# Kernel tuning notes

Hardware: AMD Instinct MI355X
Metric: run time of the kernel (lower is better)

Reference implementation:

```python
import jax, jax.numpy as jnp
import numpy as np

N_NODES = 100000
N_EDGES = 1200000
D = 64
GCN_LAYERS = 2
KEEP_PROB = 0.7


def setup_inputs() -> dict:
    key = jax.random.key(0)
    k1, k2, k3, k4, k5, k6, k7 = jax.random.split(key, 7)
    all_emb = jax.random.normal(k1, (N_NODES, D), dtype=jnp.float32)
    W = jax.random.normal(k2, (D, D), dtype=jnp.float32) * 0.05
    b = jax.random.normal(k3, (D,), dtype=jnp.float32) * 0.05
    # sparse adjacency values (e.g. normalized weights)
    vals = jax.random.uniform(k4, (N_EDGES,), dtype=jnp.float32)
    # per-layer dropout uniforms, mirrors torch.rand(len(values)) each layer
    drop_u = jax.random.uniform(k5, (GCN_LAYERS, N_EDGES), dtype=jnp.float32)
    rows = jax.random.randint(k6, (N_EDGES,), 0, N_NODES)
    cols = jax.random.randint(k7, (N_EDGES,), 0, N_NODES)
    return {"all_emb": all_emb, "W": W, "b": b, "vals": vals,
            "drop_u": drop_u, "rows": rows, "cols": cols}


def reference(all_emb, W, b, vals, drop_u, rows, cols):
    # emb[0] = fc(all_emb)
    acc = all_emb @ W.T + b  # [N, D]
    x = all_emb
    for layer in range(GCN_LAYERS):
        # edge dropout: keep iff (u + keep_prob) floors to 1, scale by 1/keep_prob
        keep = (drop_u[layer] + KEEP_PROB) >= 1.0
        v = jnp.where(keep, vals / KEEP_PROB, 0.0)  # [E]
        # SpMM: x <- A_dropped @ x via gather + segment-sum scatter
        msgs = v[:, None] * x[cols]  # [E, D]
        x = jax.ops.segment_sum(msgs, rows, num_segments=N_NODES)  # [N, D]
        acc = acc + x
    # mean over stacked (gcn_layers + 1) embeddings
    return acc / float(GCN_LAYERS + 1)
```

## Files before the change

kernel.cpp:

```cpp
#include <hip/hip_runtime.h>

#define N_NODES 100000
#define N_EDGES 1200000
#define D 64
#define KEEP_PROB 0.7f
#define INV_KEEP (1.0f / KEEP_PROB)
#define NBUCK 1564
#define MAXB 1024
#define PPART 256
#define CHUNK4 1172
#define NB64 ((NBUCK + 63) / 64)

#define ALOAD_I(p)   __hip_atomic_load((p), __ATOMIC_RELAXED, __HIP_MEMORY_SCOPE_AGENT)
#define ALOAD_U64(p) __hip_atomic_load((p), __ATOMIC_RELAXED, __HIP_MEMORY_SCOPE_AGENT)

__global__ __launch_bounds__(256) void zero_kernel(float4* __restrict__ p, int n4) {
    int i = blockIdx.x * 256 + threadIdx.x;
    if (i < n4) p[i] = make_float4(0.f, 0.f, 0.f, 0.f);
}

__global__ __launch_bounds__(256) void bucket_hist_kernel(const int4* __restrict__ rows4,
                                                          int* __restrict__ h) {
    __shared__ int hh[NBUCK];
    int p = blockIdx.x;
    int t = threadIdx.x;
    for (int i = t; i < NBUCK; i += 256) hh[i] = 0;
    __syncthreads();
    int i0 = p * CHUNK4;
    int i1 = i0 + CHUNK4;
    if (i1 > N_EDGES / 4) i1 = N_EDGES / 4;
    for (int i = i0 + t; i < i1; i += 256) {
        int4 r = rows4[i];
        atomicAdd(&hh[r.x >> 6], 1);
        atomicAdd(&hh[r.y >> 6], 1);
        atomicAdd(&hh[r.z >> 6], 1);
        atomicAdd(&hh[r.w >> 6], 1);
    }
    __syncthreads();
    int* hp = h + p * NBUCK;
    for (int i = t; i < NBUCK; i += 256) hp[i] = hh[i];
}

__global__ __launch_bounds__(256) void sum_kernel(const int* __restrict__ h,
                                                  int* __restrict__ total) {
    __shared__ int sq[4][64];
    int t = threadIdx.x;
    int bo = t & 63, q = t >> 6;
    int b = blockIdx.x * 64 + bo;
    int s = 0;
    if (b < NBUCK) {
        for (int p = q * 64; p < q * 64 + 64; ++p) s += h[p * NBUCK + b];
    }
    sq[q][bo] = s;
    __syncthreads();
    if (q == 0 && b < NBUCK)
        total[b] = sq[0][bo] + sq[1][bo] + sq[2][bo] + sq[3][bo];
}

__global__ __launch_bounds__(256) void bucket_scan_kernel(const int* __restrict__ total,
                                                          int* __restrict__ bbase) {
    __shared__ int part[256];
    const int CH = 7;
    int t = threadIdx.x;
    int e[CH]; int s = 0;
    #pragma unroll
    for (int k = 0; k < CH; ++k) {
        int j = t * CH + k;
        e[k] = (j < NBUCK) ? total[j] : 0;
        s += e[k];
    }
    part[t] = s;
    __syncthreads();
    for (int d = 1; d < 256; d <<= 1) {
        int w = (t >= d) ? part[t - d] : 0;
        __syncthreads();
        part[t] += w;
        __syncthreads();
    }
    int run = part[t] - s;
    #pragma unroll
    for (int k = 0; k < CH; ++k) {
        int j = t * CH + k;
        if (j < NBUCK) { bbase[j] = run; run += e[k]; }
    }
    if (t == 255) bbase[NBUCK] = run;
}

__global__ __launch_bounds__(256) void rebase_kernel(int* __restrict__ h,
                                                     const int* __restrict__ bbase) {
    __shared__ int sq[4][64];
    int t = threadIdx.x;
    int bo = t & 63, q = t >> 6;
    int b = blockIdx.x * 64 + bo;
    bool ok = (b < NBUCK);
    int s = 0;
    if (ok) {
        for (int p = q * 64; p < q * 64 + 64; ++p) s += h[p * NBUCK + b];
    }
    sq[q][bo] = s;
    __syncthreads();
    if (ok) {
        int run = bbase[b];
        for (int qq = 0; qq < q; ++qq) run += sq[qq][bo];
        for (int p = q * 64; p < q * 64 + 64; ++p) {
            int idx = p * NBUCK + b;
            int c = h[idx];
            h[idx] = run;
            run += c;
        }
    }
}

__global__ __launch_bounds__(256) void partition_kernel(
    const int4*   __restrict__ rows4,
    const int4*   __restrict__ cols4,
    const float4* __restrict__ vals4,
    const float4* __restrict__ u04,
    const float4* __restrict__ u14,
    const int*    __restrict__ h,
    uint4*        __restrict__ staging) {
    __shared__ int cur[NBUCK];
    int p = blockIdx.x;
    int t = threadIdx.x;
    const int* hp = h + p * NBUCK;
    for (int i = t; i < NBUCK; i += 256) cur[i] = hp[i];
    __syncthreads();

    int i0 = p * CHUNK4;
    int i1 = i0 + CHUNK4;
    if (i1 > N_EDGES / 4) i1 = N_EDGES / 4;
    for (int i = i0 + t; i < i1; i += 256) {
        int4   r  = rows4[i];
        int4   c  = cols4[i];
        float4 v  = vals4[i];
        float4 u0 = u04[i];
        float4 u1 = u14[i];

        int p0 = atomicAdd(&cur[r.x >> 6], 1);
        int p1 = atomicAdd(&cur[r.y >> 6], 1);
        int p2 = atomicAdd(&cur[r.z >> 6], 1);
        int p3 = atomicAdd(&cur[r.w >> 6], 1);

        uint4 rec; float vv;
        vv = v.x * INV_KEEP;
        rec.x = (unsigned)c.x;
        rec.y = __float_as_uint((u0.x + KEEP_PROB >= 1.0f) ? vv : 0.f);
        rec.z = __float_as_uint((u1.x + KEEP_PROB >= 1.0f) ? vv : 0.f);
        rec.w = (unsigned)r.x;
        staging[p0] = rec;
        vv = v.y * INV_KEEP;
        rec.x = (unsigned)c.y;
        rec.y = __float_as_uint((u0.y + KEEP_PROB >= 1.0f) ? vv : 0.f);
        rec.z = __float_as_uint((u1.y + KEEP_PROB >= 1.0f) ? vv : 0.f);
        rec.w = (unsigned)r.y;
        staging[p1] = rec;
        vv = v.z * INV_KEEP;
        rec.x = (unsigned)c.z;
        rec.y = __float_as_uint((u0.z + KEEP_PROB >= 1.0f) ? vv : 0.f);
        rec.z = __float_as_uint((u1.z + KEEP_PROB >= 1.0f) ? vv : 0.f);
        rec.w = (unsigned)r.z;
        staging[p2] = rec;
        vv = v.w * INV_KEEP;
        rec.x = (unsigned)c.w;
        rec.y = __float_as_uint((u0.w + KEEP_PROB >= 1.0f) ? vv : 0.f);
        rec.z = __float_as_uint((u1.w + KEEP_PROB >= 1.0f) ? vv : 0.f);
        rec.w = (unsigned)r.w;
        staging[p3] = rec;
    }
}

__global__ __launch_bounds__(256) void finalize_kernel(
    const uint4* __restrict__ staging,
    const int*   __restrict__ bbase,
    unsigned long long* __restrict__ ed0,
    unsigned long long* __restrict__ ed1) {
    __shared__ uint4 recs[MAXB];
    __shared__ int cnt[64], cur[64], part[64];
    int b = blockIdx.x;
    int t = threadIdx.x;
    int base = bbase[b];
    int size = bbase[b + 1] - base;
    bool small = (size <= MAXB);

    if (small) {
        for (int i = t; i < size; i += 256) recs[i] = staging[base + i];
    }
    if (t < 64) cnt[t] = 0;
    __syncthreads();

    for (int i = t; i < size; i += 256) {
        unsigned rw = small ? recs[i].w : staging[base + i].w;
        atomicAdd(&cnt[rw & 63], 1);
    }
    __syncthreads();

    int v = (t < 64) ? cnt[t] : 0;
    if (t < 64) part[t] = v;
    __syncthreads();
    for (int d = 1; d < 64; d <<= 1) {
        int w = (t >= d && t < 64) ? part[t - d] : 0;
        __syncthreads();
        if (t < 64) part[t] += w;
        __syncthreads();
    }
    if (t < 64) cur[t] = part[t] - v;
    __syncthreads();

    for (int i = t; i < size; i += 256) {
        uint4 r = small ? recs[i] : staging[base + i];
        unsigned lr = r.w & 63u;
        int slot = base + atomicAdd(&cur[lr], 1);
        unsigned cr = r.x | (lr << 17);
        ed0[slot] = ((unsigned long long)r.y << 32) | cr;
        ed1[slot] = ((unsigned long long)r.z << 32) | cr;
    }
}

__global__ __launch_bounds__(256) void spmm_flat_kernel(
    const float4* __restrict__ x_in,
    const unsigned long long* __restrict__ ed,
    const int*   __restrict__ bbase,
    float4*      __restrict__ io,
    int layer) {
    __shared__ float accs[64 * 64];
    __shared__ float partb[16][64];
    __shared__ int   prow[16];
    int b = blockIdx.x;
    int t = threadIdx.x;
    int base = bbase[b];
    int size = bbase[b + 1] - base;
    int row0 = b << 6;

    #pragma unroll
    for (int i = 0; i < 4; ++i)
        *(float4*)&accs[(i * 256 + t) * 4] = make_float4(0.f, 0.f, 0.f, 0.f);
    if (t < 16) prow[t] = -1;
    __syncthreads();

    int g   = t >> 4;
    int l16 = t & 15;
    int e0 = base + ((size * g) >> 4);
    int e1 = base + ((size * (g + 1)) >> 4);
    int j0 = l16 << 2;

    bool partial = false;
    if (e0 < e1 && e0 > base) {
        unsigned plo = (unsigned)ALOAD_U64(&ed[e0 - 1]);
        unsigned flo = (unsigned)ALOAD_U64(&ed[e0]);
        partial = ((plo >> 17) == (flo >> 17));
    }

    float4 acc = make_float4(0.f, 0.f, 0.f, 0.f);
    int cur = -1;
    bool first = true;
    for (int e = e0; e < e1; ++e) {
        unsigned long long rec = ALOAD_U64(&ed[e]);
        unsigned lo = (unsigned)rec;
        float v = __uint_as_float((unsigned)(rec >> 32));
        int lr = (int)(lo >> 17);
        if (lr != cur) {
            if (cur >= 0) {
                if (first && partial) {
                    *(float4*)&partb[g][j0] = acc;
                    if (l16 == 0) prow[g] = cur;
                } else {
                    *(float4*)&accs[(cur << 6) + j0] = acc;
                }
                first = false;
            }
            acc = make_float4(0.f, 0.f, 0.f, 0.f);
            cur = lr;
        }
        int c  = (int)(lo & 0x1ffffu);
        int cc = (v != 0.f) ? c : 0;
        float4 x = x_in[(cc << 4) + l16];
        acc.x = fmaf(v, x.x, acc.x);
        acc.y = fmaf(v, x.y, acc.y);
        acc.z = fmaf(v, x.z, acc.z);
        acc.w = fmaf(v, x.w, acc.w);
    }
    if (cur >= 0) {
        if (first && partial) {
            *(float4*)&partb[g][j0] = acc;
            if (l16 == 0) prow[g] = cur;
        } else {
            *(float4*)&accs[(cur << 6) + j0] = acc;
        }
    }
    __syncthreads();

    if (t < 16) {
        int jj = t << 2;
        for (int gg = 1; gg < 16; ++gg) {
            int pr = prow[gg];
            if (pr >= 0) {
                float* a = &accs[(pr << 6) + jj];
                const float* p = &partb[gg][jj];
                a[0] += p[0]; a[1] += p[1]; a[2] += p[2]; a[3] += p[3];
            }
        }
    }
    __syncthreads();

    #pragma unroll
    for (int i = 0; i < 4; ++i) {
        int idx = i * 256 + t;
        int lr = idx >> 4;
        int gg = idx & 15;
        int row = row0 + lr;
        if (row < N_NODES) {
            float4 sv = *(const float4*)&accs[(lr << 6) + (gg << 2)];
            int o = (row << 4) + gg;
            if (layer == 0) {
                io[o] = sv;
            } else {
                float4 p = io[o];
                p.x = (p.x + sv.x) * (1.0f / 3.0f);
                p.y = (p.y + sv.y) * (1.0f / 3.0f);
                p.z = (p.z + sv.z) * (1.0f / 3.0f);
                p.w = (p.w + sv.w) * (1.0f / 3.0f);
                io[o] = p;
            }
        }
    }
}

#define FMA4(A, E, WV) \
    A.x = fmaf(E, WV.x, A.x); A.y = fmaf(E, WV.y, A.y); \
    A.z = fmaf(E, WV.z, A.z); A.w = fmaf(E, WV.w, A.w);

__global__ __launch_bounds__(256, 4) void fc_add_kernel(
    const float* __restrict__ emb,
    const float* __restrict__ W,
    const float* __restrict__ b,
    const float* __restrict__ x1,
    float*       __restrict__ out) {
    __shared__ float Wt[D * 68];
    __shared__ float Es[64 * 68];

    int t = threadIdx.x;
    int n0 = blockIdx.x * 64;

    #pragma unroll
    for (int i = 0; i < 16; ++i) {
        int idx = i * 256 + t;
        Wt[(idx & 63) * 68 + (idx >> 6)] = W[idx];
    }
    #pragma unroll
    for (int i = 0; i < 4; ++i) {
        int idx4 = i * 256 + t;
        int n = idx4 >> 4;
        int k0 = (idx4 & 15) * 4;
        float4 v = make_float4(0.f, 0.f, 0.f, 0.f);
        if (n0 + n < N_NODES) v = *(const float4*)&emb[(n0 + n) * D + k0];
        *(float4*)&Es[n * 68 + k0] = v;
    }
    __syncthreads();

    int tj = t & 15;
    int tn = t >> 4;
    int j0 = tj * 4;

    float4 bb = *(const float4*)&b[j0];
    float4 acc[4];
    #pragma unroll
    for (int i = 0; i < 4; ++i) acc[i] = bb;

    const float* es = &Es[(tn * 4) * 68];
    #pragma unroll 4
    for (int kc = 0; kc < 16; ++kc) {
        int k = kc * 4;
        float4 w0 = *(const float4*)&Wt[(k + 0) * 68 + j0];
        float4 w1 = *(const float4*)&Wt[(k + 1) * 68 + j0];
        float4 w2 = *(const float4*)&Wt[(k + 2) * 68 + j0];
        float4 w3 = *(const float4*)&Wt[(k + 3) * 68 + j0];
        float4 e0 = *(const float4*)&es[0 * 68 + k];
        float4 e1 = *(const float4*)&es[1 * 68 + k];
        float4 e2 = *(const float4*)&es[2 * 68 + k];
        float4 e3 = *(const float4*)&es[3 * 68 + k];
        FMA4(acc[0], e0.x, w0); FMA4(acc[0], e0.y, w1);
        FMA4(acc[0], e0.z, w2); FMA4(acc[0], e0.w, w3);
        FMA4(acc[1], e1.x, w0); FMA4(acc[1], e1.y, w1);
        FMA4(acc[1], e1.z, w2); FMA4(acc[1], e1.w, w3);
        FMA4(acc[2], e2.x, w0); FMA4(acc[2], e2.y, w1);
        FMA4(acc[2], e2.z, w2); FMA4(acc[2], e2.w, w3);
        FMA4(acc[3], e3.x, w0); FMA4(acc[3], e3.y, w1);
        FMA4(acc[3], e3.z, w2); FMA4(acc[3], e3.w, w3);
    }

    #pragma unroll
    for (int i = 0; i < 4; ++i) {
        int n = n0 + tn * 4 + i;
        if (n < N_NODES) {
            float4 p = *(const float4*)&x1[n * D + j0];
            float4 a = acc[i];
            a.x += p.x; a.y += p.y; a.z += p.z; a.w += p.w;
            *(float4*)&out[n * D + j0] = a;
        }
    }
}

__global__ __launch_bounds__(256) void spmm_atomic_kernel(
    const float* __restrict__ x_in,
    const float* __restrict__ vals,
    const float* __restrict__ drop_u,
    const int*   __restrict__ rows,
    const int*   __restrict__ cols,
    float*       __restrict__ x_out) {
    int wave = (blockIdx.x * 256 + threadIdx.x) >> 6;
    int lane = threadIdx.x & 63;
    if (wave >= N_EDGES) return;
    float u = drop_u[wave];
    if (u + KEEP_PROB < 1.0f) return;
    float v = vals[wave] * INV_KEEP;
    atomicAdd(&x_out[rows[wave] * D + lane], v * x_in[cols[wave] * D + lane]);
}

__global__ __launch_bounds__(256) void scale_kernel(float4* __restrict__ p, int n4) {
    int i = blockIdx.x * 256 + threadIdx.x;
    if (i < n4) {
        float4 v = p[i];
        v.x *= (1.f/3.f); v.y *= (1.f/3.f); v.z *= (1.f/3.f); v.w *= (1.f/3.f);
        p[i] = v;
    }
}

extern "C" void kernel_launch(void* const* d_in, const int* in_sizes, int n_in,
                              void* d_out, int out_size, void* d_ws, size_t ws_size,
                              hipStream_t stream) {
    const float* all_emb = (const float*)d_in[0];
    const float* W       = (const float*)d_in[1];
    const float* b       = (const float*)d_in[2];
    const float* vals    = (const float*)d_in[3];
    const float* drop_u  = (const float*)d_in[4];
    const int*   rows    = (const int*)d_in[5];
    const int*   cols    = (const int*)d_in[6];

    float* out = (float*)d_out;

    char* ws = (char*)d_ws;
    float* x1       = (float*)(ws);
    uint4* staging  = (uint4*)(ws);
    int*   h        = (int*)  (ws + 19200000);
    unsigned long long* ed0 = (unsigned long long*)(ws + 26000064);
    unsigned long long* ed1 = (unsigned long long*)(ws + 35600064);
    int*   total    = (int*)  (ws + 45200064);
    int*   bbase    = (int*)  (ws + 45206320);
    const size_t WS_NEEDED = 45406528;

    const int n4 = N_NODES * D / 4;
    const int zb = (n4 + 255) / 256;
    const int fc_blocks = (N_NODES + 63) / 64;

    if (ws_size >= WS_NEEDED) {
        bucket_hist_kernel<<<PPART, 256, 0, stream>>>((const int4*)rows, h);
        sum_kernel<<<NB64, 256, 0, stream>>>(h, total);
        bucket_scan_kernel<<<1, 256, 0, stream>>>(total, bbase);
        rebase_kernel<<<NB64, 256, 0, stream>>>(h, bbase);
        partition_kernel<<<PPART, 256, 0, stream>>>(
            (const int4*)rows, (const int4*)cols, (const float4*)vals,
            (const float4*)drop_u, (const float4*)(drop_u + N_EDGES),
            h, staging);
        finalize_kernel<<<NBUCK, 256, 0, stream>>>(staging, bbase, ed0, ed1);
        spmm_flat_kernel<<<NBUCK, 256, 0, stream>>>(
            (const float4*)all_emb, ed0, bbase, (float4*)x1, 0);
        fc_add_kernel<<<fc_blocks, 256, 0, stream>>>(all_emb, W, b, x1, out);
        spmm_flat_kernel<<<NBUCK, 256, 0, stream>>>(
            (const float4*)x1, ed1, bbase, (float4*)out, 1);
    } else {
        const int spmm_blocks = (N_EDGES + 3) / 4;
        zero_kernel<<<zb, 256, 0, stream>>>((float4*)x1, n4);
        spmm_atomic_kernel<<<spmm_blocks, 256, 0, stream>>>(all_emb, vals, drop_u,
                                                            rows, cols, x1);
        fc_add_kernel<<<fc_blocks, 256, 0, stream>>>(all_emb, W, b, x1, out);
        spmm_atomic_kernel<<<spmm_blocks, 256, 0, stream>>>(x1, vals,
                                                            drop_u + N_EDGES,
                                                            rows, cols, out);
        scale_kernel<<<zb, 256, 0, stream>>>((float4*)out, n4);
    }
}
```

Before: 271.2 us.

## Fuse per-bucket row sort into SpMM kernel and drop finalize pass

```diff
diff --git a/kernel.cpp b/kernel.cpp
--- a/kernel.cpp
+++ b/kernel.cpp
@@ -118,7 +118,8 @@
     const float4* __restrict__ u04,
     const float4* __restrict__ u14,
     const int*    __restrict__ h,
-    uint4*        __restrict__ staging) {
+    unsigned long long* __restrict__ s0,
+    unsigned long long* __restrict__ s1) {
     __shared__ int cur[NBUCK];
     int p = blockIdx.x;
     int t = threadIdx.x;
@@ -141,90 +142,44 @@
         int p2 = atomicAdd(&cur[r.z >> 6], 1);
         int p3 = atomicAdd(&cur[r.w >> 6], 1);
 
-        uint4 rec; float vv;
+        float vv; unsigned cr, v0b, v1b;
         vv = v.x * INV_KEEP;
-        rec.x = (unsigned)c.x;
-        rec.y = __float_as_uint((u0.x + KEEP_PROB >= 1.0f) ? vv : 0.f);
-        rec.z = __float_as_uint((u1.x + KEEP_PROB >= 1.0f) ? vv : 0.f);
-        rec.w = (unsigned)r.x;
-        staging[p0] = rec;
+        cr = (unsigned)c.x | (((unsigned)r.x & 63u) << 17);
+        v0b = __float_as_uint((u0.x + KEEP_PROB >= 1.0f) ? vv : 0.f);
+        v1b = __float_as_uint((u1.x + KEEP_PROB >= 1.0f) ? vv : 0.f);
+        s0[p0] = ((unsigned long long)v0b << 32) | cr;
+        s1[p0] = ((unsigned long long)v1b << 32) | cr;
         vv = v.y * INV_KEEP;
-        rec.x = (unsigned)c.y;
-        rec.y = __float_as_uint((u0.y + KEEP_PROB >= 1.0f) ? vv : 0.f);
-        rec.z = __float_as_uint((u1.y + KEEP_PROB >= 1.0f) ? vv : 0.f);
-        rec.w = (unsigned)r.y;
-        staging[p1] = rec;
+        cr = (unsigned)c.y | (((unsigned)r.y & 63u) << 17);
+        v0b = __float_as_uint((u0.y + KEEP_PROB >= 1.0f) ? vv : 0.f);
+        v1b = __float_as_uint((u1.y + KEEP_PROB >= 1.0f) ? vv : 0.f);
+        s0[p1] = ((unsigned long long)v0b << 32) | cr;
+        s1[p1] = ((unsigned long long)v1b << 32) | cr;
         vv = v.z * INV_KEEP;
-        rec.x = (unsigned)c.z;
-        rec.y = __float_as_uint((u0.z + KEEP_PROB >= 1.0f) ? vv : 0.f);
-        rec.z = __float_as_uint((u1.z + KEEP_PROB >= 1.0f) ? vv : 0.f);
-        rec.w = (unsigned)r.z;
-        staging[p2] = rec;
+        cr = (unsigned)c.z | (((unsigned)r.z & 63u) << 17);
+        v0b = __float_as_uint((u0.z + KEEP_PROB >= 1.0f) ? vv : 0.f);
+        v1b = __float_as_uint((u1.z + KEEP_PROB >= 1.0f) ? vv : 0.f);
+        s0[p2] = ((unsigned long long)v0b << 32) | cr;
+        s1[p2] = ((unsigned long long)v1b << 32) | cr;
         vv = v.w * INV_KEEP;
-        rec.x = (unsigned)c.w;
-        rec.y = __float_as_uint((u0.w + KEEP_PROB >= 1.0f) ? vv : 0.f);
-        rec.z = __float_as_uint((u1.w + KEEP_PROB >= 1.0f) ? vv : 0.f);
-        rec.w = (unsigned)r.w;
-        staging[p3] = rec;
-    }
-}
-
-__global__ __launch_bounds__(256) void finalize_kernel(
-    const uint4* __restrict__ staging,
-    const int*   __restrict__ bbase,
-    unsigned long long* __restrict__ ed0,
-    unsigned long long* __restrict__ ed1) {
-    __shared__ uint4 recs[MAXB];
-    __shared__ int cnt[64], cur[64], part[64];
-    int b = blockIdx.x;
-    int t = threadIdx.x;
-    int base = bbase[b];
-    int size = bbase[b + 1] - base;
-    bool small = (size <= MAXB);
-
-    if (small) {
-        for (int i = t; i < size; i += 256) recs[i] = staging[base + i];
-    }
-    if (t < 64) cnt[t] = 0;
-    __syncthreads();
-
-    for (int i = t; i < size; i += 256) {
-        unsigned rw = small ? recs[i].w : staging[base + i].w;
-        atomicAdd(&cnt[rw & 63], 1);
-    }
-    __syncthreads();
-
-    int v = (t < 64) ? cnt[t] : 0;
-    if (t < 64) part[t] = v;
-    __syncthreads();
-    for (int d = 1; d < 64; d <<= 1) {
-        int w = (t >= d && t < 64) ? part[t - d] : 0;
-        __syncthreads();
-        if (t < 64) part[t] += w;
-        __syncthreads();
-    }
-    if (t < 64) cur[t] = part[t] - v;
-    __syncthreads();
-
-    for (int i = t; i < size; i += 256) {
-        uint4 r = small ? recs[i] : staging[base + i];
-        unsigned lr = r.w & 63u;
-        int slot = base + atomicAdd(&cur[lr], 1);
-        unsigned cr = r.x | (lr << 17);
-        ed0[slot] = ((unsigned long long)r.y << 32) | cr;
-        ed1[slot] = ((unsigned long long)r.z << 32) | cr;
-    }
-}
-
-__global__ __launch_bounds__(256) void spmm_flat_kernel(
+        cr = (unsigned)c.w | (((unsigned)r.w & 63u) << 17);
+        v0b = __float_as_uint((u0.w + KEEP_PROB >= 1.0f) ? vv : 0.f);
+        v1b = __float_as_uint((u1.w + KEEP_PROB >= 1.0f) ? vv : 0.f);
+        s0[p3] = ((unsigned long long)v0b << 32) | cr;
+        s1[p3] = ((unsigned long long)v1b << 32) | cr;
+    }
+}
+
+__global__ __launch_bounds__(256) void spmm_sort_kernel(
     const float4* __restrict__ x_in,
-    const unsigned long long* __restrict__ ed,
+    const unsigned long long* __restrict__ s,
     const int*   __restrict__ bbase,
     float4*      __restrict__ io,
     int layer) {
     __shared__ float accs[64 * 64];
+    __shared__ unsigned long long sl[MAXB];
     __shared__ float partb[16][64];
-    __shared__ int   prow[16];
+    __shared__ int cnt[64], cur[64], pref[64], prow[16];
     int b = blockIdx.x;
     int t = threadIdx.x;
     int base = bbase[b];
@@ -234,73 +189,106 @@
     #pragma unroll
     for (int i = 0; i < 4; ++i)
         *(float4*)&accs[(i * 256 + t) * 4] = make_float4(0.f, 0.f, 0.f, 0.f);
-    if (t < 16) prow[t] = -1;
     __syncthreads();
 
     int g   = t >> 4;
     int l16 = t & 15;
-    int e0 = base + ((size * g) >> 4);
-    int e1 = base + ((size * (g + 1)) >> 4);
-    int j0 = l16 << 2;
-
-    bool partial = false;
-    if (e0 < e1 && e0 > base) {
-        unsigned plo = (unsigned)ALOAD_U64(&ed[e0 - 1]);
-        unsigned flo = (unsigned)ALOAD_U64(&ed[e0]);
-        partial = ((plo >> 17) == (flo >> 17));
-    }
-
-    float4 acc = make_float4(0.f, 0.f, 0.f, 0.f);
-    int cur = -1;
-    bool first = true;
-    for (int e = e0; e < e1; ++e) {
-        unsigned long long rec = ALOAD_U64(&ed[e]);
-        unsigned lo = (unsigned)rec;
-        float v = __uint_as_float((unsigned)(rec >> 32));
-        int lr = (int)(lo >> 17);
-        if (lr != cur) {
-            if (cur >= 0) {
-                if (first && partial) {
-                    *(float4*)&partb[g][j0] = acc;
-                    if (l16 == 0) prow[g] = cur;
-                } else {
-                    *(float4*)&accs[(cur << 6) + j0] = acc;
+    int j0  = l16 << 2;
+
+    for (int c0 = 0; c0 < size; c0 += MAXB) {
+        int csize = size - c0; if (csize > MAXB) csize = MAXB;
+        if (t < 64) cnt[t] = 0;
+        if (t < 16) prow[t] = -1;
+        __syncthreads();
+        for (int i = t; i < csize; i += 256) {
+            unsigned lo = (unsigned)ALOAD_U64(&s[base + c0 + i]);
+            atomicAdd(&cnt[lo >> 17], 1);
+        }
+        __syncthreads();
+        int v = (t < 64) ? cnt[t] : 0;
+        if (t < 64) pref[t] = v;
+        __syncthreads();
+        for (int d = 1; d < 64; d <<= 1) {
+            int w = (t >= d && t < 64) ? pref[t - d] : 0;
+            __syncthreads();
+            if (t < 64) pref[t] += w;
+            __syncthreads();
+        }
+        if (t < 64) cur[t] = pref[t] - v;
+        __syncthreads();
+        for (int i = t; i < csize; i += 256) {
+            unsigned long long rec = ALOAD_U64(&s[base + c0 + i]);
+            int lr = (int)((unsigned)rec >> 17);
+            int slot = atomicAdd(&cur[lr], 1);
+            sl[slot] = rec;
+        }
+        __syncthreads();
+
+        int e0 = (csize * g) >> 4;
+        int e1 = (csize * (g + 1)) >> 4;
+        bool partial = false;
+        if (e0 < e1 && e0 > 0) {
+            unsigned plo = (unsigned)sl[e0 - 1];
+            unsigned flo = (unsigned)sl[e0];
+            partial = ((plo >> 17) == (flo >> 17));
+        }
+        float4 acc = make_float4(0.f, 0.f, 0.f, 0.f);
+        int curR = -1;
+        bool first = true;
+        for (int e = e0; e < e1; ++e) {
+            unsigned long long rec = sl[e];
+            unsigned lo = (unsigned)rec;
+            float vv = __uint_as_float((unsigned)(rec >> 32));
+            int lr = (int)(lo >> 17);
+            if (lr != curR) {
+                if (curR >= 0) {
+                    if (first && partial) {
+                        *(float4*)&partb[g][j0] = acc;
+                        if (l16 == 0) prow[g] = curR;
+                    } else {
+                        float4* p = (float4*)&accs[(curR << 6) + j0];
+                        float4 o = *p;
+                        o.x += acc.x; o.y += acc.y; o.z += acc.z; o.w += acc.w;
+                        *p = o;
+                    }
+                    first = false;
                 }
-                first = false;
+                acc = make_float4(0.f, 0.f, 0.f, 0.f);
+                curR = lr;
             }
-            acc = make_float4(0.f, 0.f, 0.f, 0.f);
-            cur = lr;
-        }
-        int c  = (int)(lo & 0x1ffffu);
-        int cc = (v != 0.f) ? c : 0;
-        float4 x = x_in[(cc << 4) + l16];
-        acc.x = fmaf(v, x.x, acc.x);
-        acc.y = fmaf(v, x.y, acc.y);
-        acc.z = fmaf(v, x.z, acc.z);
-        acc.w = fmaf(v, x.w, acc.w);
-    }
-    if (cur >= 0) {
-        if (first && partial) {
-            *(float4*)&partb[g][j0] = acc;
-            if (l16 == 0) prow[g] = cur;
-        } else {
-            *(float4*)&accs[(cur << 6) + j0] = acc;
-        }
-    }
-    __syncthreads();
-
-    if (t < 16) {
-        int jj = t << 2;
-        for (int gg = 1; gg < 16; ++gg) {
-            int pr = prow[gg];
-            if (pr >= 0) {
-                float* a = &accs[(pr << 6) + jj];
-                const float* p = &partb[gg][jj];
-                a[0] += p[0]; a[1] += p[1]; a[2] += p[2]; a[3] += p[3];
+            int c  = (int)(lo & 0x1ffffu);
+            int cc = (vv != 0.f) ? c : 0;
+            float4 x = x_in[(cc << 4) + l16];
+            acc.x = fmaf(vv, x.x, acc.x);
+            acc.y = fmaf(vv, x.y, acc.y);
+            acc.z = fmaf(vv, x.z, acc.z);
+            acc.w = fmaf(vv, x.w, acc.w);
+        }
+        if (curR >= 0) {
+            if (first && partial) {
+                *(float4*)&partb[g][j0] = acc;
+                if (l16 == 0) prow[g] = curR;
+            } else {
+                float4* p = (float4*)&accs[(curR << 6) + j0];
+                float4 o = *p;
+                o.x += acc.x; o.y += acc.y; o.z += acc.z; o.w += acc.w;
+                *p = o;
             }
         }
-    }
-    __syncthreads();
+        __syncthreads();
+        if (t < 16) {
+            int jj = t << 2;
+            for (int gg = 1; gg < 16; ++gg) {
+                int pr = prow[gg];
+                if (pr >= 0) {
+                    float* a = &accs[(pr << 6) + jj];
+                    const float* p = &partb[gg][jj];
+                    a[0] += p[0]; a[1] += p[1]; a[2] += p[2]; a[3] += p[3];
+                }
+            }
+        }
+        __syncthreads();
+    }
 
     #pragma unroll
     for (int i = 0; i < 4; ++i) {
@@ -440,10 +428,9 @@
 
     char* ws = (char*)d_ws;
     float* x1       = (float*)(ws);
-    uint4* staging  = (uint4*)(ws);
     int*   h        = (int*)  (ws + 19200000);
-    unsigned long long* ed0 = (unsigned long long*)(ws + 26000064);
-    unsigned long long* ed1 = (unsigned long long*)(ws + 35600064);
+    unsigned long long* s0 = (unsigned long long*)(ws + 26000064);
+    unsigned long long* s1 = (unsigned long long*)(ws + 35600064);
     int*   total    = (int*)  (ws + 45200064);
     int*   bbase    = (int*)  (ws + 45206320);
     const size_t WS_NEEDED = 45406528;
@@ -460,13 +447,12 @@
         partition_kernel<<<PPART, 256, 0, stream>>>(
             (const int4*)rows, (const int4*)cols, (const float4*)vals,
             (const float4*)drop_u, (const float4*)(drop_u + N_EDGES),
-            h, staging);
-        finalize_kernel<<<NBUCK, 256, 0, stream>>>(staging, bbase, ed0, ed1);
-        spmm_flat_kernel<<<NBUCK, 256, 0, stream>>>(
-            (const float4*)all_emb, ed0, bbase, (float4*)x1, 0);
+            h, s0, s1);
+        spmm_sort_kernel<<<NBUCK, 256, 0, stream>>>(
+            (const float4*)all_emb, s0, bbase, (float4*)x1, 0);
         fc_add_kernel<<<fc_blocks, 256, 0, stream>>>(all_emb, W, b, x1, out);
-        spmm_flat_kernel<<<NBUCK, 256, 0, stream>>>(
-            (const float4*)x1, ed1, bbase, (float4*)out, 1);
+        spmm_sort_kernel<<<NBUCK, 256, 0, stream>>>(
+            (const float4*)x1, s1, bbase, (float4*)out, 1);
     } else {
         const int spmm_blocks = (N_EDGES + 3) / 4;
         zero_kernel<<<zb, 256, 0, stream>>>((float4*)x1, n4);
```

Result: slower. 286.5 us (+5.7%).
